# Kernel optimization log

Measured on AMD Instinct MI355X. Metric: run time of the kernel, lower is better.

The kernel has to match this reference:

```python
import jax, jax.numpy as jnp
import numpy as np

EPS = 1e-6
DELTA = 1e-6
GAMMA = 1.0


def setup_inputs() -> dict:
    key = jax.random.key(0)
    ks = jax.random.split(key, 6)
    B, N, D, DDIR, DSIM = 2, 384, 256, 128, 64
    sc = lambda d: 1.0 / np.sqrt(d)
    return {
        "t": jax.random.normal(ks[0], (B, N, D), jnp.float32),
        "Qd": jax.random.normal(ks[1], (D, DDIR), jnp.float32) * sc(D),
        "Kd": jax.random.normal(ks[2], (D, DDIR), jnp.float32) * sc(D),
        "Vd": jax.random.normal(ks[3], (DDIR, D), jnp.float32) * sc(DDIR),
        "Qs": jax.random.normal(ks[4], (D, DSIM), jnp.float32) * sc(D),
        "Ks": jax.random.normal(ks[5], (D, DSIM), jnp.float32) * sc(D),
        "a_l": jnp.ones((1,), jnp.float32),
        "b_l": jnp.zeros((1,), jnp.float32),
    }


def reference(t, Qd, Kd, Vd, Qs, Ks, a_l, b_l):
    B, N, D = t.shape
    d_sim = Qs.shape[1]
    # --- similarity: s_ij = <Qs t_i, Ks t_j>/sqrt(d_sim), then symmetrize ---
    q = t @ Qs  # (B,N,d_sim)
    k = t @ Ks
    s = jnp.einsum('bnd,bmd->bnm', q, k) / jnp.sqrt(jnp.float32(d_sim))
    s = 0.5 * (s + s.transpose(0, 2, 1))
    # --- global z-score over off-diagonal entries (biased var) ---
    eye = jnp.eye(N, dtype=bool)[None]  # (1,N,N)
    cnt = jnp.float32(N * (N - 1))
    mu = jnp.where(eye, 0.0, s).sum((1, 2), keepdims=True) / cnt  # (B,1,1)
    var = jnp.where(eye, 0.0, (s - mu) ** 2).sum((1, 2), keepdims=True) / cnt
    s_hat = (s - mu) / jnp.sqrt(var + EPS)
    tilde_s = a_l.reshape(-1, 1, 1) * s_hat + b_l.reshape(-1, 1, 1)
    # --- gates / mass / inertia / apportioned step ---
    A = jax.nn.sigmoid(tilde_s)                                  # (B,N,N)
    m = 1.0 / (jnp.exp(GAMMA * tilde_s).sum(axis=2) + EPS)       # (B,N)
    w = A * m[:, None, :]                                        # w_ij = m_j A_ij
    alpha = A * (w / (w.sum(axis=2, keepdims=True) + DELTA))     # (B,N,N)
    # --- antisymmetric Hadamard direction gate ---
    qd = t @ Qd  # (B,N,d_dir)
    kd = t @ Kd
    had = qd[:, :, None, :] * kd[:, None, :, :]                  # (B,N,N,d_dir)
    kappa = jnp.einsum('bijr,rd->bijd', had, Vd)                 # (B,N,N,D)
    gate = jax.nn.sigmoid(kappa - kappa.transpose(0, 2, 1, 3))
    Dpair = gate * (t[:, :, None, :] - t[:, None, :, :])         # D_ij = gate*(t_i - t_j)
    # --- exclude self pairs, aggregate update ---
    off = ~eye  # (1,N,N)
    alpha = jnp.where(off, alpha, 0.0)
    Dpair = jnp.where(off[..., None], Dpair, 0.0)
    t_next = t - jnp.einsum('bnm,bnmd->bnd', alpha, Dpair)
    return t_next
```

## Files before the change

### kernel.cpp

```cpp
#include <hip/hip_runtime.h>

#define Bn 2
#define Nn 384
#define Dn 256
#define Rn 128
#define Sn 64
#define BNn (Bn*Nn)
#define NEG_LOG2E -1.44269504088896f

typedef short short8 __attribute__((ext_vector_type(8)));
typedef float f32x4 __attribute__((ext_vector_type(4)));
typedef unsigned int uint;
typedef unsigned short ushort;

static __device__ __forceinline__ float fast_sigmoid(float x) {
    return __builtin_amdgcn_rcpf(1.0f + __expf(-x));
}
static __device__ __forceinline__ ushort f2bf(float f) {
    uint u = __float_as_uint(f);
    uint r = (u + 0x7fffu + ((u >> 16) & 1u)) >> 16;
    return (ushort)r;
}
static __device__ __forceinline__ float bf2f(ushort u) {
    return __uint_as_float(((uint)u) << 16);
}

__global__ __launch_bounds__(256)
void prep_kernel(const float* __restrict__ t,
                 const float* __restrict__ Qd, const float* __restrict__ Kd,
                 const float* __restrict__ Vd,
                 const float* __restrict__ Qs, const float* __restrict__ Ks,
                 float* __restrict__ q, float* __restrict__ k,
                 ushort* __restrict__ qdb, ushort* __restrict__ kdb,
                 ushort* __restrict__ VdT, float* __restrict__ stats) {
    const int bi = blockIdx.x;
    const int tid = threadIdx.x;
    if (bi >= 192) {
        const int idx = (bi - 192) * 256 + tid;
        const int d = idx >> 7, r = idx & 127;
        VdT[idx] = f2bf(NEG_LOG2E * Vd[(size_t)r * Dn + d]);
        if (bi == 319 && tid < 4) stats[tid] = 0.0f;
        return;
    }
    __shared__ float trow[4][Dn];
    const int r0 = bi * 4;
    for (int idx = tid; idx < 4 * Dn; idx += 256)
        trow[idx >> 8][idx & 255] = t[(size_t)r0 * Dn + idx];
    __syncthreads();
    {
        const float* W = (tid < 128) ? Qd : Kd;
        ushort* ob = (tid < 128) ? qdb : kdb;
        const int col = tid & 127;
        float a0 = 0.f, a1 = 0.f, a2 = 0.f, a3 = 0.f;
        for (int kk = 0; kk < Dn; kk += 4) {
            float4 t0 = *(const float4*)&trow[0][kk];
            float4 t1 = *(const float4*)&trow[1][kk];
            float4 t2 = *(const float4*)&trow[2][kk];
            float4 t3 = *(const float4*)&trow[3][kk];
            float w0 = W[(size_t)(kk + 0) * 128 + col];
            float w1 = W[(size_t)(kk + 1) * 128 + col];
            float w2 = W[(size_t)(kk + 2) * 128 + col];
            float w3 = W[(size_t)(kk + 3) * 128 + col];
            a0 += t0.x * w0 + t0.y * w1 + t0.z * w2 + t0.w * w3;
            a1 += t1.x * w0 + t1.y * w1 + t1.z * w2 + t1.w * w3;
            a2 += t2.x * w0 + t2.y * w1 + t2.z * w2 + t2.w * w3;
            a3 += t3.x * w0 + t3.y * w1 + t3.z * w2 + t3.w * w3;
        }
        ob[(size_t)(r0 + 0) * 128 + col] = f2bf(a0);
        ob[(size_t)(r0 + 1) * 128 + col] = f2bf(a1);
        ob[(size_t)(r0 + 2) * 128 + col] = f2bf(a2);
        ob[(size_t)(r0 + 3) * 128 + col] = f2bf(a3);
    }
    if (tid < 128) {
        const float* W = (tid < 64) ? Qs : Ks;
        float* of = (tid < 64) ? q : k;
        const int col = tid & 63;
        float a0 = 0.f, a1 = 0.f, a2 = 0.f, a3 = 0.f;
        for (int kk = 0; kk < Dn; kk += 4) {
            float4 t0 = *(const float4*)&trow[0][kk];
            float4 t1 = *(const float4*)&trow[1][kk];
            float4 t2 = *(const float4*)&trow[2][kk];
            float4 t3 = *(const float4*)&trow[3][kk];
            float w0 = W[(size_t)(kk + 0) * 64 + col];
            float w1 = W[(size_t)(kk + 1) * 64 + col];
            float w2 = W[(size_t)(kk + 2) * 64 + col];
            float w3 = W[(size_t)(kk + 3) * 64 + col];
            a0 += t0.x * w0 + t0.y * w1 + t0.z * w2 + t0.w * w3;
            a1 += t1.x * w0 + t1.y * w1 + t1.z * w2 + t1.w * w3;
            a2 += t2.x * w0 + t2.y * w1 + t2.z * w2 + t2.w * w3;
            a3 += t3.x * w0 + t3.y * w1 + t3.z * w2 + t3.w * w3;
        }
        of[(size_t)(r0 + 0) * 64 + col] = a0;
        of[(size_t)(r0 + 1) * 64 + col] = a1;
        of[(size_t)(r0 + 2) * 64 + col] = a2;
        of[(size_t)(r0 + 3) * 64 + col] = a3;
    }
}

__global__ __launch_bounds__(256)
void ssym_kernel(const float* __restrict__ q, const float* __restrict__ k,
                 float* __restrict__ ssym, float* __restrict__ stats) {
    __shared__ float qi[16][68], ki[16][68], qj[16][68], kj[16][68];
    __shared__ float red[256];
    const int b = blockIdx.z, it = blockIdx.x, jt = blockIdx.y;
    const int tid = threadIdx.x;
    const int r0 = tid >> 6, c = tid & 63;
#pragma unroll
    for (int p = 0; p < 4; ++p) {
        int row = r0 + 4 * p;
        qi[row][c] = q[((size_t)(b * Nn + it * 16 + row)) * Sn + c];
        ki[row][c] = k[((size_t)(b * Nn + it * 16 + row)) * Sn + c];
        qj[row][c] = q[((size_t)(b * Nn + jt * 16 + row)) * Sn + c];
        kj[row][c] = k[((size_t)(b * Nn + jt * 16 + row)) * Sn + c];
    }
    __syncthreads();
    const int ti = tid >> 4, tj = tid & 15;
    float acc = 0.0f;
#pragma unroll
    for (int dd = 0; dd < Sn; dd += 4) {
        float4 a  = *(const float4*)&qi[ti][dd];
        float4 bb = *(const float4*)&kj[tj][dd];
        float4 cc = *(const float4*)&qj[tj][dd];
        float4 d  = *(const float4*)&ki[ti][dd];
        acc += a.x * bb.x + a.y * bb.y + a.z * bb.z + a.w * bb.w
             + cc.x * d.x + cc.y * d.y + cc.z * d.z + cc.w * d.w;
    }
    const float sval = acc * 0.0625f;
    const int gi = it * 16 + ti, gj = jt * 16 + tj;
    ssym[((size_t)(b * Nn + gi)) * Nn + gj] = sval;
    const float v = (gi == gj) ? 0.0f : sval;

    red[tid] = v;
    __syncthreads();
    for (int off = 128; off > 0; off >>= 1) {
        if (tid < off) red[tid] += red[tid + off];
        __syncthreads();
    }
    const float tot_s = red[0];
    __syncthreads();
    red[tid] = v * v;
    __syncthreads();
    for (int off = 128; off > 0; off >>= 1) {
        if (tid < off) red[tid] += red[tid + off];
        __syncthreads();
    }
    if (tid == 0) {
        atomicAdd(&stats[b * 2 + 0], tot_s);
        atomicAdd(&stats[b * 2 + 1], red[0]);
    }
}

__global__ __launch_bounds__(256)
void m_kernel(const float* __restrict__ ssym, const float* __restrict__ stats,
              const float* __restrict__ a_l, const float* __restrict__ b_l,
              float* __restrict__ m) {
    __shared__ float red[256];
    const int row = blockIdx.x;
    const int b = row / Nn;
    const float cnt_inv = 1.0f / (float)(Nn * (Nn - 1));
    const float mu = stats[b * 2 + 0] * cnt_inv;
    const float var = stats[b * 2 + 1] * cnt_inv - mu * mu;
    const float isg = rsqrtf(var + 1e-6f);
    const float a = a_l[0], bbias = b_l[0];
    const int tid = threadIdx.x;
    float sum = __expf(a * (ssym[(size_t)row * Nn + tid] - mu) * isg + bbias);
    if (tid < 128)
        sum += __expf(a * (ssym[(size_t)row * Nn + 256 + tid] - mu) * isg + bbias);
    red[tid] = sum;
    __syncthreads();
    for (int off = 128; off > 0; off >>= 1) {
        if (tid < off) red[tid] += red[tid + off];
        __syncthreads();
    }
    if (tid == 0) m[row] = 1.0f / (red[0] + 1e-6f);
}

__global__ __launch_bounds__(256, 3)
void pair_kernel(const float* __restrict__ t, const float* __restrict__ ssym,
                 const float* __restrict__ mptr, const float* __restrict__ stats,
                 const float* __restrict__ a_l, const float* __restrict__ b_l,
                 const ushort* __restrict__ qdb, const ushort* __restrict__ kdb,
                 const ushort* __restrict__ VdT, float* __restrict__ out) {
    __shared__ ushort h_s[128][136];
    __shared__ float alpha_s[Nn];
    __shared__ float qdi_s[Rn], kdi_s[Rn];
    __shared__ float red[256];

    const int bi = blockIdx.x;
    const int b = bi / Nn;
    const int i = bi - b * Nn;
    const int tid = threadIdx.x;
    const int wave = tid >> 6, lane = tid & 63;
    const int ln = lane & 15, quad = lane >> 4;
    const int wd0 = wave * 64;

    {
        const float cnt_inv = 1.0f / (float)(Nn * (Nn - 1));
        const float mu = stats[b * 2 + 0] * cnt_inv;
        const float var = stats[b * 2 + 1] * cnt_inv - mu * mu;
        const float isg = rsqrtf(var + 1e-6f);
        const float a = a_l[0], bbias = b_l[0];
        float A0, am0, A1 = 0.f, am1 = 0.f;
        {
            float s0 = ssym[(size_t)bi * Nn + tid];
            A0 = fast_sigmoid(a * (s0 - mu) * isg + bbias);
            am0 = A0 * mptr[b * Nn + tid];
        }
        if (tid < 128) {
            float s1 = ssym[(size_t)bi * Nn + 256 + tid];
            A1 = fast_sigmoid(a * (s1 - mu) * isg + bbias);
            am1 = A1 * mptr[b * Nn + 256 + tid];
        }
        red[tid] = am0 + am1;
        __syncthreads();
        for (int off = 128; off > 0; off >>= 1) {
            if (tid < off) red[tid] += red[tid + off];
            __syncthreads();
        }
        const float inv = 1.0f / (red[0] + 1e-6f);
        alpha_s[tid] = (tid == i) ? 0.f : A0 * am0 * inv;
        if (tid < 128)
            alpha_s[256 + tid] = ((256 + tid) == i) ? 0.f : A1 * am1 * inv;
    }
    if (tid < Rn) {
        qdi_s[tid] = bf2f(qdb[(size_t)bi * Rn + tid]);
        kdi_s[tid] = bf2f(kdb[(size_t)bi * Rn + tid]);
    }

    short8 vf[4][4];
#pragma unroll
    for (int dt = 0; dt < 4; ++dt)
#pragma unroll
        for (int ks = 0; ks < 4; ++ks)
            vf[dt][ks] = *(const short8*)&VdT[(size_t)(wd0 + dt * 16 + ln) * Rn + ks * 32 + quad * 8];

    float4 tiv[4];
#pragma unroll
    for (int dt = 0; dt < 4; ++dt)
        tiv[dt] = *(const float4*)&t[(size_t)bi * Dn + wd0 + dt * 16 + quad * 4];

    float4 outac[4];
#pragma unroll
    for (int dt = 0; dt < 4; ++dt) outac[dt] = make_float4(0.f, 0.f, 0.f, 0.f);

    for (int jt0 = 0; jt0 < Nn; jt0 += 128) {
        __syncthreads();
        {
            const int jj = tid >> 1;
            const int r0s = (tid & 1) * 64;
            const size_t rowj = (size_t)(b * Nn + jt0 + jj) * Rn;
            const uint4* qp = (const uint4*)(qdb + rowj + r0s);
            const uint4* kp = (const uint4*)(kdb + rowj + r0s);
#pragma unroll
            for (int c = 0; c < 8; ++c) {
                uint4 qv = qp[c], kv = kp[c];
                uint pk[4];
#pragma unroll
                for (int p = 0; p < 4; ++p) {
                    uint qu = (&qv.x)[p], ku = (&kv.x)[p];
                    float qlo = __uint_as_float(qu << 16);
                    float qhi = __uint_as_float(qu & 0xffff0000u);
                    float klo = __uint_as_float(ku << 16);
                    float khi = __uint_as_float(ku & 0xffff0000u);
                    const int r = r0s + c * 8 + p * 2;
                    float h0 = qdi_s[r]     * klo - kdi_s[r]     * qlo;
                    float h1 = qdi_s[r + 1] * khi - kdi_s[r + 1] * qhi;
                    pk[p] = (uint)f2bf(h0) | ((uint)f2bf(h1) << 16);
                }
                uint4 w; w.x = pk[0]; w.y = pk[1]; w.z = pk[2]; w.w = pk[3];
                *(uint4*)&h_s[jj][r0s + c * 8] = w;
            }
        }
        __syncthreads();

#pragma unroll 1
        for (int jsub = 0; jsub < 8; ++jsub) {
            short8 hf[4];
#pragma unroll
            for (int ks = 0; ks < 4; ++ks)
                hf[ks] = *(const short8*)&h_s[jsub * 16 + ln][ks * 32 + quad * 8];
            const int j = jt0 + jsub * 16 + ln;
            const float al = alpha_s[j];
            const size_t trow_ = (size_t)(b * Nn + j) * Dn;
            float4 tjv[4];
#pragma unroll
            for (int dt = 0; dt < 4; ++dt)
                tjv[dt] = *(const float4*)&t[trow_ + wd0 + dt * 16 + quad * 4];

            f32x4 aA[4], aB[4];
#pragma unroll
            for (int dt = 0; dt < 4; ++dt) {
                f32x4 x = {0.f, 0.f, 0.f, 0.f}, y = {0.f, 0.f, 0.f, 0.f};
                x = __builtin_amdgcn_mfma_f32_16x16x32_bf16(vf[dt][0], hf[0], x, 0, 0, 0);
                y = __builtin_amdgcn_mfma_f32_16x16x32_bf16(vf[dt][1], hf[1], y, 0, 0, 0);
                x = __builtin_amdgcn_mfma_f32_16x16x32_bf16(vf[dt][2], hf[2], x, 0, 0, 0);
                y = __builtin_amdgcn_mfma_f32_16x16x32_bf16(vf[dt][3], hf[3], y, 0, 0, 0);
                aA[dt] = x; aB[dt] = y;
            }
#pragma unroll
            for (int dt = 0; dt < 4; ++dt) {
                const float4 tj = tjv[dt];
                float e0 = aA[dt][0] + aB[dt][0];
                float e1 = aA[dt][1] + aB[dt][1];
                float e2 = aA[dt][2] + aB[dt][2];
                float e3 = aA[dt][3] + aB[dt][3];
                float g0 = __builtin_amdgcn_rcpf(1.0f + __builtin_amdgcn_exp2f(e0));
                float g1 = __builtin_amdgcn_rcpf(1.0f + __builtin_amdgcn_exp2f(e1));
                float g2 = __builtin_amdgcn_rcpf(1.0f + __builtin_amdgcn_exp2f(e2));
                float g3 = __builtin_amdgcn_rcpf(1.0f + __builtin_amdgcn_exp2f(e3));
                outac[dt].x += al * g0 * (tiv[dt].x - tj.x);
                outac[dt].y += al * g1 * (tiv[dt].y - tj.y);
                outac[dt].z += al * g2 * (tiv[dt].z - tj.z);
                outac[dt].w += al * g3 * (tiv[dt].w - tj.w);
            }
        }
    }

#pragma unroll
    for (int dt = 0; dt < 4; ++dt) {
        float4 v = outac[dt];
#pragma unroll
        for (int mask = 1; mask < 16; mask <<= 1) {
            v.x += __shfl_xor(v.x, mask);
            v.y += __shfl_xor(v.y, mask);
            v.z += __shfl_xor(v.z, mask);
            v.w += __shfl_xor(v.w, mask);
        }
        if (ln == 0) {
            float4 o;
            o.x = tiv[dt].x - v.x;
            o.y = tiv[dt].y - v.y;
            o.z = tiv[dt].z - v.z;
            o.w = tiv[dt].w - v.w;
            *(float4*)&out[(size_t)bi * Dn + wd0 + dt * 16 + quad * 4] = o;
        }
    }
}

extern "C" void kernel_launch(void* const* d_in, const int* in_sizes, int n_in,
                              void* d_out, int out_size, void* d_ws, size_t ws_size,
                              hipStream_t stream) {
    const float* t   = (const float*)d_in[0];
    const float* Qd  = (const float*)d_in[1];
    const float* Kd  = (const float*)d_in[2];
    const float* Vd  = (const float*)d_in[3];
    const float* Qs  = (const float*)d_in[4];
    const float* Ks  = (const float*)d_in[5];
    const float* a_l = (const float*)d_in[6];
    const float* b_l = (const float*)d_in[7];
    float* out = (float*)d_out;
    float* ws  = (float*)d_ws;

    float* q     = ws;
    float* k     = q + BNn * Sn;
    float* ssym  = k + BNn * Sn;
    float* m     = ssym + (size_t)BNn * Nn;
    float* stats = m + BNn;
    ushort* qdb  = (ushort*)(stats + 8);
    ushort* kdb  = qdb + (size_t)BNn * Rn;
    ushort* VdT  = kdb + (size_t)BNn * Rn;

    hipLaunchKernelGGL(prep_kernel, dim3(320), dim3(256), 0, stream,
                       t, Qd, Kd, Vd, Qs, Ks, q, k, qdb, kdb, VdT, stats);
    hipLaunchKernelGGL(ssym_kernel, dim3(Nn / 16, Nn / 16, Bn), dim3(256), 0, stream,
                       q, k, ssym, stats);
    hipLaunchKernelGGL(m_kernel, dim3(BNn), dim3(256), 0, stream, ssym, stats, a_l, b_l, m);
    hipLaunchKernelGGL(pair_kernel, dim3(BNn), dim3(256), 0, stream,
                       t, ssym, m, stats, a_l, b_l, qdb, kdb, VdT, out);
}
```

Measured before the change: 186.6 us.

## Split pair kernel across D halves, precompute alpha in separate kernel, use shuffle reductions

Moves the alpha computation out of pair_kernel into a new alpha_kernel that writes alpha to global workspace. pair_kernel now launches two blocks per row, each handling half of D, with a smaller j-tile of 64 and launch bounds allowing 6 blocks per CU. The aim is more parallelism and occupancy in the dominant kernel. The shared-memory tree reductions in ssym, m and alpha are replaced with wave shuffles. The trade-off is an extra launch, an alpha round trip through global memory, and the Hadamard tile being rebuilt twice per row.

```diff
diff --git a/kernel.cpp b/kernel.cpp
--- a/kernel.cpp
+++ b/kernel.cpp
@@ -6,6 +6,7 @@
 #define Rn 128
 #define Sn 64
 #define BNn (Bn*Nn)
+#define JT 64
 #define NEG_LOG2E -1.44269504088896f
 
 typedef short short8 __attribute__((ext_vector_type(8)));
@@ -101,7 +102,7 @@
 void ssym_kernel(const float* __restrict__ q, const float* __restrict__ k,
                  float* __restrict__ ssym, float* __restrict__ stats) {
     __shared__ float qi[16][68], ki[16][68], qj[16][68], kj[16][68];
-    __shared__ float red[256];
+    __shared__ float part[8];
     const int b = blockIdx.z, it = blockIdx.x, jt = blockIdx.y;
     const int tid = threadIdx.x;
     const int r0 = tid >> 6, c = tid & 63;
@@ -130,23 +131,18 @@
     ssym[((size_t)(b * Nn + gi)) * Nn + gj] = sval;
     const float v = (gi == gj) ? 0.0f : sval;
 
-    red[tid] = v;
-    __syncthreads();
-    for (int off = 128; off > 0; off >>= 1) {
-        if (tid < off) red[tid] += red[tid + off];
-        __syncthreads();
-    }
-    const float tot_s = red[0];
-    __syncthreads();
-    red[tid] = v * v;
-    __syncthreads();
-    for (int off = 128; off > 0; off >>= 1) {
-        if (tid < off) red[tid] += red[tid + off];
-        __syncthreads();
-    }
+    float vs = v, v2 = v * v;
+#pragma unroll
+    for (int mask = 32; mask > 0; mask >>= 1) {
+        vs += __shfl_xor(vs, mask);
+        v2 += __shfl_xor(v2, mask);
+    }
+    const int lane = tid & 63, wave = tid >> 6;
+    if (lane == 0) { part[wave] = vs; part[4 + wave] = v2; }
+    __syncthreads();
     if (tid == 0) {
-        atomicAdd(&stats[b * 2 + 0], tot_s);
-        atomicAdd(&stats[b * 2 + 1], red[0]);
+        atomicAdd(&stats[b * 2 + 0], part[0] + part[1] + part[2] + part[3]);
+        atomicAdd(&stats[b * 2 + 1], part[4] + part[5] + part[6] + part[7]);
     }
 }
 
@@ -154,7 +150,7 @@
 void m_kernel(const float* __restrict__ ssym, const float* __restrict__ stats,
               const float* __restrict__ a_l, const float* __restrict__ b_l,
               float* __restrict__ m) {
-    __shared__ float red[256];
+    __shared__ float part[4];
     const int row = blockIdx.x;
     const int b = row / Nn;
     const float cnt_inv = 1.0f / (float)(Nn * (Nn - 1));
@@ -166,93 +162,99 @@
     float sum = __expf(a * (ssym[(size_t)row * Nn + tid] - mu) * isg + bbias);
     if (tid < 128)
         sum += __expf(a * (ssym[(size_t)row * Nn + 256 + tid] - mu) * isg + bbias);
-    red[tid] = sum;
-    __syncthreads();
-    for (int off = 128; off > 0; off >>= 1) {
-        if (tid < off) red[tid] += red[tid + off];
-        __syncthreads();
-    }
-    if (tid == 0) m[row] = 1.0f / (red[0] + 1e-6f);
-}
-
-__global__ __launch_bounds__(256, 3)
-void pair_kernel(const float* __restrict__ t, const float* __restrict__ ssym,
-                 const float* __restrict__ mptr, const float* __restrict__ stats,
-                 const float* __restrict__ a_l, const float* __restrict__ b_l,
+#pragma unroll
+    for (int mask = 32; mask > 0; mask >>= 1) sum += __shfl_xor(sum, mask);
+    if ((tid & 63) == 0) part[tid >> 6] = sum;
+    __syncthreads();
+    if (tid == 0) m[row] = 1.0f / (part[0] + part[1] + part[2] + part[3] + 1e-6f);
+}
+
+__global__ __launch_bounds__(256)
+void alpha_kernel(const float* __restrict__ ssym, const float* __restrict__ stats,
+                  const float* __restrict__ mptr,
+                  const float* __restrict__ a_l, const float* __restrict__ b_l,
+                  float* __restrict__ alpha) {
+    __shared__ float part[4];
+    const int row = blockIdx.x;
+    const int b = row / Nn;
+    const int i = row - b * Nn;
+    const float cnt_inv = 1.0f / (float)(Nn * (Nn - 1));
+    const float mu = stats[b * 2 + 0] * cnt_inv;
+    const float var = stats[b * 2 + 1] * cnt_inv - mu * mu;
+    const float isg = rsqrtf(var + 1e-6f);
+    const float a = a_l[0], bbias = b_l[0];
+    const int tid = threadIdx.x;
+    float A0, am0, A1 = 0.f, am1 = 0.f;
+    {
+        float s0 = ssym[(size_t)row * Nn + tid];
+        A0 = fast_sigmoid(a * (s0 - mu) * isg + bbias);
+        am0 = A0 * mptr[b * Nn + tid];
+    }
+    if (tid < 128) {
+        float s1 = ssym[(size_t)row * Nn + 256 + tid];
+        A1 = fast_sigmoid(a * (s1 - mu) * isg + bbias);
+        am1 = A1 * mptr[b * Nn + 256 + tid];
+    }
+    float sum = am0 + am1;
+#pragma unroll
+    for (int mask = 32; mask > 0; mask >>= 1) sum += __shfl_xor(sum, mask);
+    if ((tid & 63) == 0) part[tid >> 6] = sum;
+    __syncthreads();
+    const float inv = 1.0f / (part[0] + part[1] + part[2] + part[3] + 1e-6f);
+    alpha[(size_t)row * Nn + tid] = (tid == i) ? 0.f : A0 * am0 * inv;
+    if (tid < 128)
+        alpha[(size_t)row * Nn + 256 + tid] = ((256 + tid) == i) ? 0.f : A1 * am1 * inv;
+}
+
+__global__ __launch_bounds__(256, 6)
+void pair_kernel(const float* __restrict__ t, const float* __restrict__ alpha,
                  const ushort* __restrict__ qdb, const ushort* __restrict__ kdb,
                  const ushort* __restrict__ VdT, float* __restrict__ out) {
-    __shared__ ushort h_s[128][136];
-    __shared__ float alpha_s[Nn];
+    __shared__ ushort h_s[JT][136];
     __shared__ float qdi_s[Rn], kdi_s[Rn];
-    __shared__ float red[256];
-
-    const int bi = blockIdx.x;
+
+    const int blk = blockIdx.x;
+    const int bi = blk >> 1;
+    const int dh = blk & 1;
     const int b = bi / Nn;
-    const int i = bi - b * Nn;
     const int tid = threadIdx.x;
     const int wave = tid >> 6, lane = tid & 63;
     const int ln = lane & 15, quad = lane >> 4;
-    const int wd0 = wave * 64;
-
-    {
-        const float cnt_inv = 1.0f / (float)(Nn * (Nn - 1));
-        const float mu = stats[b * 2 + 0] * cnt_inv;
-        const float var = stats[b * 2 + 1] * cnt_inv - mu * mu;
-        const float isg = rsqrtf(var + 1e-6f);
-        const float a = a_l[0], bbias = b_l[0];
-        float A0, am0, A1 = 0.f, am1 = 0.f;
-        {
-            float s0 = ssym[(size_t)bi * Nn + tid];
-            A0 = fast_sigmoid(a * (s0 - mu) * isg + bbias);
-            am0 = A0 * mptr[b * Nn + tid];
-        }
-        if (tid < 128) {
-            float s1 = ssym[(size_t)bi * Nn + 256 + tid];
-            A1 = fast_sigmoid(a * (s1 - mu) * isg + bbias);
-            am1 = A1 * mptr[b * Nn + 256 + tid];
-        }
-        red[tid] = am0 + am1;
-        __syncthreads();
-        for (int off = 128; off > 0; off >>= 1) {
-            if (tid < off) red[tid] += red[tid + off];
-            __syncthreads();
-        }
-        const float inv = 1.0f / (red[0] + 1e-6f);
-        alpha_s[tid] = (tid == i) ? 0.f : A0 * am0 * inv;
-        if (tid < 128)
-            alpha_s[256 + tid] = ((256 + tid) == i) ? 0.f : A1 * am1 * inv;
-    }
+    const int wd0 = dh * 128 + wave * 32;
+
     if (tid < Rn) {
         qdi_s[tid] = bf2f(qdb[(size_t)bi * Rn + tid]);
         kdi_s[tid] = bf2f(kdb[(size_t)bi * Rn + tid]);
     }
 
-    short8 vf[4][4];
-#pragma unroll
-    for (int dt = 0; dt < 4; ++dt)
+    short8 vf[2][4];
+#pragma unroll
+    for (int dt = 0; dt < 2; ++dt)
 #pragma unroll
         for (int ks = 0; ks < 4; ++ks)
             vf[dt][ks] = *(const short8*)&VdT[(size_t)(wd0 + dt * 16 + ln) * Rn + ks * 32 + quad * 8];
 
-    float4 tiv[4];
-#pragma unroll
-    for (int dt = 0; dt < 4; ++dt)
+    float4 tiv[2];
+#pragma unroll
+    for (int dt = 0; dt < 2; ++dt)
         tiv[dt] = *(const float4*)&t[(size_t)bi * Dn + wd0 + dt * 16 + quad * 4];
 
-    float4 outac[4];
-#pragma unroll
-    for (int dt = 0; dt < 4; ++dt) outac[dt] = make_float4(0.f, 0.f, 0.f, 0.f);
-
-    for (int jt0 = 0; jt0 < Nn; jt0 += 128) {
+    float4 outac[2];
+#pragma unroll
+    for (int dt = 0; dt < 2; ++dt) outac[dt] = make_float4(0.f, 0.f, 0.f, 0.f);
+
+    const float* alpr = alpha + (size_t)bi * Nn;
+
+    for (int jt0 = 0; jt0 < Nn; jt0 += JT) {
         __syncthreads();
         {
-            const int jj = tid >> 1;
-            const int r0s = (tid & 1) * 64;
+            const int jj = tid >> 2;
+            const int r0s = (tid & 3) * 32;
             const size_t rowj = (size_t)(b * Nn + jt0 + jj) * Rn;
             const uint4* qp = (const uint4*)(qdb + rowj + r0s);
             const uint4* kp = (const uint4*)(kdb + rowj + r0s);
 #pragma unroll
-            for (int c = 0; c < 8; ++c) {
+            for (int c = 0; c < 4; ++c) {
                 uint4 qv = qp[c], kv = kp[c];
                 uint pk[4];
 #pragma unroll
@@ -274,22 +276,22 @@
         __syncthreads();
 
 #pragma unroll 1
-        for (int jsub = 0; jsub < 8; ++jsub) {
+        for (int jsub = 0; jsub < 4; ++jsub) {
             short8 hf[4];
 #pragma unroll
             for (int ks = 0; ks < 4; ++ks)
                 hf[ks] = *(const short8*)&h_s[jsub * 16 + ln][ks * 32 + quad * 8];
             const int j = jt0 + jsub * 16 + ln;
-            const float al = alpha_s[j];
+            const float al = alpr[j];
             const size_t trow_ = (size_t)(b * Nn + j) * Dn;
-            float4 tjv[4];
-#pragma unroll
-            for (int dt = 0; dt < 4; ++dt)
+            float4 tjv[2];
+#pragma unroll
+            for (int dt = 0; dt < 2; ++dt)
                 tjv[dt] = *(const float4*)&t[trow_ + wd0 + dt * 16 + quad * 4];
 
-            f32x4 aA[4], aB[4];
-#pragma unroll
-            for (int dt = 0; dt < 4; ++dt) {
+            f32x4 aA[2], aB[2];
+#pragma unroll
+            for (int dt = 0; dt < 2; ++dt) {
                 f32x4 x = {0.f, 0.f, 0.f, 0.f}, y = {0.f, 0.f, 0.f, 0.f};
                 x = __builtin_amdgcn_mfma_f32_16x16x32_bf16(vf[dt][0], hf[0], x, 0, 0, 0);
                 y = __builtin_amdgcn_mfma_f32_16x16x32_bf16(vf[dt][1], hf[1], y, 0, 0, 0);
@@ -298,7 +300,7 @@
                 aA[dt] = x; aB[dt] = y;
             }
 #pragma unroll
-            for (int dt = 0; dt < 4; ++dt) {
+            for (int dt = 0; dt < 2; ++dt) {
                 const float4 tj = tjv[dt];
                 float e0 = aA[dt][0] + aB[dt][0];
                 float e1 = aA[dt][1] + aB[dt][1];
@@ -317,7 +319,7 @@
     }
 
 #pragma unroll
-    for (int dt = 0; dt < 4; ++dt) {
+    for (int dt = 0; dt < 2; ++dt) {
         float4 v = outac[dt];
 #pragma unroll
         for (int mask = 1; mask < 16; mask <<= 1) {
@@ -359,12 +361,15 @@
     ushort* qdb  = (ushort*)(stats + 8);
     ushort* kdb  = qdb + (size_t)BNn * Rn;
     ushort* VdT  = kdb + (size_t)BNn * Rn;
+    float* alpha = (float*)(VdT + (size_t)Dn * Rn);
 
     hipLaunchKernelGGL(prep_kernel, dim3(320), dim3(256), 0, stream,
                        t, Qd, Kd, Vd, Qs, Ks, q, k, qdb, kdb, VdT, stats);
     hipLaunchKernelGGL(ssym_kernel, dim3(Nn / 16, Nn / 16, Bn), dim3(256), 0, stream,
                        q, k, ssym, stats);
     hipLaunchKernelGGL(m_kernel, dim3(BNn), dim3(256), 0, stream, ssym, stats, a_l, b_l, m);
-    hipLaunchKernelGGL(pair_kernel, dim3(BNn), dim3(256), 0, stream,
-                       t, ssym, m, stats, a_l, b_l, qdb, kdb, VdT, out);
-}
+    hipLaunchKernelGGL(alpha_kernel, dim3(BNn), dim3(256), 0, stream,
+                       ssym, stats, m, a_l, b_l, alpha);
+    hipLaunchKernelGGL(pair_kernel, dim3(BNn * 2), dim3(256), 0, stream,
+                       t, alpha, qdb, kdb, VdT, out);
+}
```

New measurement: 306.7 us. 64.4% more time.
